# Optimization experiments

Hardware: AMD Instinct MI355X
Metric: run time of the kernel (lower is better)

The kernel has to match this reference:

```python
import jax, jax.numpy as jnp
import numpy as np

IM_SIZE = (256, 256)
OVERSAMP = 1.25
WIDTH = 6
BETA = float(np.pi * np.sqrt((WIDTH / OVERSAMP * (OVERSAMP - 0.5)) ** 2 - 0.8))
OS_SIZE = tuple(int(np.ceil(OVERSAMP * n)) for n in IM_SIZE)  # (320, 320)
D = 2


def _kb(x):
    # Kaiser-Bessel interpolation kernel: i0(beta*sqrt(1-x^2)) for |x|<=1 (sigpy convention)
    return jnp.i0(BETA * jnp.sqrt(jnp.maximum(1.0 - x * x, 0.0)))


def setup_inputs() -> dict:
    key = jax.random.key(0)
    k1, k2, k3 = jax.random.split(key, 3)
    N, C = 1, 8
    img_r = jax.random.normal(k1, (N, C) + IM_SIZE, dtype=jnp.float32)
    img_i = jax.random.normal(k2, (N, C) + IM_SIZE, dtype=jnp.float32)
    # trajectory in [-N_i/2, N_i/2] per the class docstring
    trj = (jax.random.uniform(k3, (N, 64, 4096, D), dtype=jnp.float32) - 0.5) * 256.0
    return {"img_r": img_r, "img_i": img_i, "trj": trj}


def _nufft_forward(img_r, img_i, trj):
    img = (img_r + 1j * img_i).astype(jnp.complex64)  # (N, C, H, W)
    nd = img.ndim
    # --- apodization (inverse FT of KB kernel), separable per axis ---
    for a in range(D):
        n, osn = IM_SIZE[a], OS_SIZE[a]
        idx = jnp.arange(n, dtype=jnp.float32)
        arg = jnp.sqrt(BETA ** 2 - (np.pi * WIDTH * (idx - n // 2) / osn) ** 2)
        apod = arg / jnp.sinh(arg)
        shape = [1] * nd
        shape[nd - D + a] = n
        img = img * apod.reshape(shape)
    # --- scale + centered zero-pad to oversampled grid ---
    img = img / np.sqrt(float(np.prod(IM_SIZE)))
    pads = [(0, 0)] * (nd - D) + [(((o - n) // 2), (o - n) - ((o - n) // 2))
                                  for n, o in zip(IM_SIZE, OS_SIZE)]
    img = jnp.pad(img, pads)
    # --- centered FFT (ifftshift -> fftn(norm=None) -> fftshift) ---
    axes = tuple(range(-D, 0))
    ksp_os = jnp.fft.fftshift(jnp.fft.fftn(jnp.fft.ifftshift(img, axes=axes), axes=axes), axes=axes)
    # --- scale trajectory to oversampled grid coordinates ---
    scale = jnp.array([OS_SIZE[a] / IM_SIZE[a] for a in range(D)], jnp.float32)
    shift = jnp.array([OS_SIZE[a] // 2 for a in range(D)], jnp.float32)
    coord = trj * scale + shift  # (N, R, S, 2)
    x0 = jnp.ceil(coord - WIDTH / 2.0)
    # --- KB interpolation: fixed 6x6 neighbor loop, vectorized gather over all points ---
    N = img.shape[0]
    out = jnp.zeros((N,) + img.shape[1:nd - D] + coord.shape[1:-1], jnp.complex64)

    def gather(grid, ix, iy):  # grid (C, Hos, Wos), ix/iy (R, S) -> (C, R, S)
        return grid[:, ix, iy]

    for dx in range(WIDTH):
        px = x0[..., 0] + dx
        wx = _kb((px - coord[..., 0]) / (WIDTH / 2.0))
        ix = px.astype(jnp.int32) % OS_SIZE[0]
        for dy in range(WIDTH):
            py = x0[..., 1] + dy
            wy = _kb((py - coord[..., 1]) / (WIDTH / 2.0))
            iy = py.astype(jnp.int32) % OS_SIZE[1]
            vals = jax.vmap(gather)(ksp_os, ix, iy)  # (N, C, R, S)
            out = out + vals * (wx * wy)[:, None, :, :]
    return out / (WIDTH ** D)


def reference(img_r, img_i, trj):
    return _nufft_forward(img_r, img_i, trj)
```

## Files before the change

### kernel.cpp

```cpp
#include <hip/hip_runtime.h>
#include <math.h>

#define NCH   8
#define IMN   256
#define OSN   320
#define NPTS  (64*4096)
#define KD    512
#define BETA_F   10.9551078f
#define BETA2_F  120.014389f
#define APOD_C   0.05890486225f

typedef unsigned short u16;
typedef unsigned int   u32;
typedef __attribute__((ext_vector_type(8))) short s16x8;
typedef __attribute__((ext_vector_type(4))) float f32x4;

__device__ __forceinline__ u32 f2bf(float f) {
    u32 u = __float_as_uint(f);
    return (u + 0x7FFFu + ((u >> 16) & 1u)) >> 16;
}

__device__ __forceinline__ float i0f(float t) {
    if (t < 3.75f) {
        float y = t * t * (1.0f / 14.0625f);
        return 1.0f + y * (3.5156229f + y * (3.0899424f + y * (1.2067492f +
                     y * (0.2659732f + y * (0.0360768f + y * 0.0045813f)))));
    }
    float z = 3.75f / t;
    float p = 0.39894228f + z * (0.01328592f + z * (0.00225319f + z * (-0.00157565f +
              z * (0.00916281f + z * (-0.02057706f + z * (0.02635537f +
              z * (-0.01647633f + z * 0.00392377f)))))));
    return expf(t) * rsqrtf(t) * p;
}

__device__ __forceinline__ float apodf(int i) {
    float x = APOD_C * (float)(i - IMN / 2);
    float arg = sqrtf(BETA2_F - x * x);
    float e = expf(arg);
    float sh = 0.5f * (e - 1.0f / e);
    return arg / sh;
}

__global__ void prep(const float* __restrict__ r, const float* __restrict__ im,
                     u32* __restrict__ B1, u32* __restrict__ B2,
                     u32* __restrict__ A) {
    const int b = blockIdx.x, t = threadIdx.x;
    if (b < (OSN * IMN) / 256) {
        int idx = b * 256 + t;
        int k = idx >> 8, j = idx & 255;
        int p = (k * (j + 32)) % OSN;
        float th = (2.0f * (float)M_PI / (float)OSN) * (float)p;
        float s = ((k + j) & 1) ? -1.0f : 1.0f;
        float sn, cs;
        sincosf(th, &sn, &cs);
        float re = s * cs, imv = -s * sn;
        B1[idx] = f2bf(re) | (f2bf(-imv) << 16);
        B2[idx] = f2bf(imv) | (f2bf(re) << 16);
    } else {
        int idx = (b - (OSN * IMN) / 256) * 256 + t;
        int i2 = idx & 255, i1 = (idx >> 8) & 255;
        float w = apodf(i1) * apodf(i2) * (1.0f / 256.0f);
        A[idx] = f2bf(r[idx] * w) | (f2bf(im[idx] * w) << 16);
    }
}

__launch_bounds__(64)
__global__ void gemm1(const short* __restrict__ Abf, const short* __restrict__ B1,
                      const short* __restrict__ B2, short* __restrict__ Tb) {
    const int c = blockIdx.z;
    const int mBase = blockIdx.y * 32;
    const int nBase = blockIdx.x * 32;
    __shared__ short As[2][32][36], B1s[2][32][36], B2s[2][32][36];
    const int t = threadIdx.x;
    const int row = t >> 1, seg = (t & 1) * 16;
    const int fm = t & 15, fq = (t >> 4) * 8;
    const short* ap  = Abf + (long)(c * IMN + mBase + row) * KD + seg;
    const short* b1p = B1 + (long)(nBase + row) * KD + seg;
    const short* b2p = B2 + (long)(nBase + row) * KD + seg;
    f32x4 zz = {0.f, 0.f, 0.f, 0.f};
    f32x4 accRe[2][2], accIm[2][2];
    #pragma unroll
    for (int i = 0; i < 2; i++)
        #pragma unroll
        for (int j = 0; j < 2; j++) { accRe[i][j] = zz; accIm[i][j] = zz; }

    s16x8 c0 = *(const s16x8*)(ap);
    s16x8 c1 = *(const s16x8*)(ap + 8);
    s16x8 c2 = *(const s16x8*)(b1p);
    s16x8 c3 = *(const s16x8*)(b1p + 8);
    s16x8 c4 = *(const s16x8*)(b2p);
    s16x8 c5 = *(const s16x8*)(b2p + 8);

    #pragma unroll
    for (int kc = 0; kc < 16; kc++) {
        const int buf = kc & 1;
        *(s16x8*)&As [buf][row][seg]     = c0;
        *(s16x8*)&As [buf][row][seg + 8] = c1;
        *(s16x8*)&B1s[buf][row][seg]     = c2;
        *(s16x8*)&B1s[buf][row][seg + 8] = c3;
        *(s16x8*)&B2s[buf][row][seg]     = c4;
        *(s16x8*)&B2s[buf][row][seg + 8] = c5;
        if (kc < 15) {
            const int kb = (kc + 1) * 32;
            c0 = *(const s16x8*)(ap + kb);
            c1 = *(const s16x8*)(ap + kb + 8);
            c2 = *(const s16x8*)(b1p + kb);
            c3 = *(const s16x8*)(b1p + kb + 8);
            c4 = *(const s16x8*)(b2p + kb);
            c5 = *(const s16x8*)(b2p + kb + 8);
        }
        s16x8 a0  = *(const s16x8*)&As [buf][fm][fq];
        s16x8 a1  = *(const s16x8*)&As [buf][16 + fm][fq];
        s16x8 b10 = *(const s16x8*)&B1s[buf][fm][fq];
        s16x8 b11 = *(const s16x8*)&B1s[buf][16 + fm][fq];
        s16x8 b20 = *(const s16x8*)&B2s[buf][fm][fq];
        s16x8 b21 = *(const s16x8*)&B2s[buf][16 + fm][fq];
        accRe[0][0] = __builtin_amdgcn_mfma_f32_16x16x32_bf16(a0, b10, accRe[0][0], 0, 0, 0);
        accRe[0][1] = __builtin_amdgcn_mfma_f32_16x16x32_bf16(a0, b11, accRe[0][1], 0, 0, 0);
        accRe[1][0] = __builtin_amdgcn_mfma_f32_16x16x32_bf16(a1, b10, accRe[1][0], 0, 0, 0);
        accRe[1][1] = __builtin_amdgcn_mfma_f32_16x16x32_bf16(a1, b11, accRe[1][1], 0, 0, 0);
        accIm[0][0] = __builtin_amdgcn_mfma_f32_16x16x32_bf16(a0, b20, accIm[0][0], 0, 0, 0);
        accIm[0][1] = __builtin_amdgcn_mfma_f32_16x16x32_bf16(a0, b21, accIm[0][1], 0, 0, 0);
        accIm[1][0] = __builtin_amdgcn_mfma_f32_16x16x32_bf16(a1, b20, accIm[1][0], 0, 0, 0);
        accIm[1][1] = __builtin_amdgcn_mfma_f32_16x16x32_bf16(a1, b21, accIm[1][1], 0, 0, 0);
    }
    #pragma unroll
    for (int i = 0; i < 2; i++)
        #pragma unroll
        for (int j = 0; j < 2; j++) {
            int i1b = mBase + i * 16 + (t >> 4) * 4;
            int k2  = nBase + j * 16 + fm;
            s16x8 v;
            #pragma unroll
            for (int r = 0; r < 4; r++) {
                v[2 * r]     = (short)f2bf(accRe[i][j][r]);
                v[2 * r + 1] = (short)f2bf(accIm[i][j][r]);
            }
            *(s16x8*)(Tb + ((long)(c * OSN + k2)) * KD + 2 * i1b) = v;
        }
}

__launch_bounds__(64)
__global__ void gemm2(const short* __restrict__ B1, const short* __restrict__ B2,
                      const short* __restrict__ Tb, u32* __restrict__ Gb) {
    const int c = blockIdx.z;
    const int mBase = blockIdx.y * 32;
    const int nBase = blockIdx.x * 32;
    __shared__ short A1s[2][32][36], A2s[2][32][36], Bs[2][32][36];
    const int t = threadIdx.x;
    const int row = t >> 1, seg = (t & 1) * 16;
    const int fm = t & 15, fq = (t >> 4) * 8;
    const short* a1p = B1 + (long)(mBase + row) * KD + seg;
    const short* a2p = B2 + (long)(mBase + row) * KD + seg;
    const short* bp  = Tb + ((long)(c * OSN + nBase + row)) * KD + seg;
    f32x4 zz = {0.f, 0.f, 0.f, 0.f};
    f32x4 accRe[2][2], accIm[2][2];
    #pragma unroll
    for (int i = 0; i < 2; i++)
        #pragma unroll
        for (int j = 0; j < 2; j++) { accRe[i][j] = zz; accIm[i][j] = zz; }

    s16x8 c0 = *(const s16x8*)(a1p);
    s16x8 c1 = *(const s16x8*)(a1p + 8);
    s16x8 c2 = *(const s16x8*)(a2p);
    s16x8 c3 = *(const s16x8*)(a2p + 8);
    s16x8 c4 = *(const s16x8*)(bp);
    s16x8 c5 = *(const s16x8*)(bp + 8);

    #pragma unroll
    for (int kc = 0; kc < 16; kc++) {
        const int buf = kc & 1;
        *(s16x8*)&A1s[buf][row][seg]     = c0;
        *(s16x8*)&A1s[buf][row][seg + 8] = c1;
        *(s16x8*)&A2s[buf][row][seg]     = c2;
        *(s16x8*)&A2s[buf][row][seg + 8] = c3;
        *(s16x8*)&Bs [buf][row][seg]     = c4;
        *(s16x8*)&Bs [buf][row][seg + 8] = c5;
        if (kc < 15) {
            const int kb = (kc + 1) * 32;
            c0 = *(const s16x8*)(a1p + kb);
            c1 = *(const s16x8*)(a1p + kb + 8);
            c2 = *(const s16x8*)(a2p + kb);
            c3 = *(const s16x8*)(a2p + kb + 8);
            c4 = *(const s16x8*)(bp + kb);
            c5 = *(const s16x8*)(bp + kb + 8);
        }
        s16x8 a10 = *(const s16x8*)&A1s[buf][fm][fq];
        s16x8 a11 = *(const s16x8*)&A1s[buf][16 + fm][fq];
        s16x8 a20 = *(const s16x8*)&A2s[buf][fm][fq];
        s16x8 a21 = *(const s16x8*)&A2s[buf][16 + fm][fq];
        s16x8 b0  = *(const s16x8*)&Bs [buf][fm][fq];
        s16x8 b1  = *(const s16x8*)&Bs [buf][16 + fm][fq];
        accRe[0][0] = __builtin_amdgcn_mfma_f32_16x16x32_bf16(a10, b0, accRe[0][0], 0, 0, 0);
        accRe[0][1] = __builtin_amdgcn_mfma_f32_16x16x32_bf16(a10, b1, accRe[0][1], 0, 0, 0);
        accRe[1][0] = __builtin_amdgcn_mfma_f32_16x16x32_bf16(a11, b0, accRe[1][0], 0, 0, 0);
        accRe[1][1] = __builtin_amdgcn_mfma_f32_16x16x32_bf16(a11, b1, accRe[1][1], 0, 0, 0);
        accIm[0][0] = __builtin_amdgcn_mfma_f32_16x16x32_bf16(a20, b0, accIm[0][0], 0, 0, 0);
        accIm[0][1] = __builtin_amdgcn_mfma_f32_16x16x32_bf16(a20, b1, accIm[0][1], 0, 0, 0);
        accIm[1][0] = __builtin_amdgcn_mfma_f32_16x16x32_bf16(a21, b0, accIm[1][0], 0, 0, 0);
        accIm[1][1] = __builtin_amdgcn_mfma_f32_16x16x32_bf16(a21, b1, accIm[1][1], 0, 0, 0);
    }
    #pragma unroll
    for (int i = 0; i < 2; i++)
        #pragma unroll
        for (int j = 0; j < 2; j++) {
            int k2 = nBase + j * 16 + fm;
            #pragma unroll
            for (int r = 0; r < 4; r++) {
                int k1 = mBase + i * 16 + (t >> 4) * 4 + r;
                Gb[((long)k1 * OSN + k2) * NCH + c] =
                    f2bf(accRe[i][j][r]) | (f2bf(accIm[i][j][r]) << 16);
            }
        }
}

__global__ void interp_kernel(const float* __restrict__ trj,
                              const u32* __restrict__ grid,
                              u32* __restrict__ out) {
    const int t = threadIdx.x;
    const int pl = t >> 2;
    const int cp = (t & 3) * 2;
    __shared__ float wxs[64][6], wys[64][6];
    __shared__ int   x0s[64], y0s[64];

    #pragma unroll
    for (int k = 0; k < 3; k++) {
        int e = t + 256 * k;
        int ptl = e / 12;
        int rem = e - ptl * 12;
        int axis = rem >= 6 ? 1 : 0;
        int d = rem - axis * 6;
        int pt = blockIdx.x * 64 + ptl;
        float tv = trj[pt * 2 + axis];
        float cc = __fadd_rn(__fmul_rn(tv, 1.25f), 160.0f);
        float v0 = ceilf(__fadd_rn(cc, -3.0f));
        if (d == 0) {
            if (axis) y0s[ptl] = (int)v0; else x0s[ptl] = (int)v0;
        }
        float u = __fdiv_rn(__fsub_rn(v0 + (float)d, cc), 3.0f);
        float wv = i0f(BETA_F * sqrtf(fmaxf(1.0f - u * u, 0.0f)));
        if (axis) wys[ptl][d] = wv; else wxs[ptl][d] = wv;
    }
    __syncthreads();

    int ix[6], iy[6];
    const int x0i = x0s[pl], y0i = y0s[pl];
    #pragma unroll
    for (int d = 0; d < 6; d++) {
        int vx = x0i + d;
        ix[d] = ((vx % OSN) + OSN) % OSN;
        int vy = y0i + d;
        iy[d] = ((vy % OSN) + OSN) % OSN;
    }

    float re0 = 0.f, im0 = 0.f, re1 = 0.f, im1 = 0.f;
    #pragma unroll
    for (int dx = 0; dx < 6; dx++) {
        long base = (long)ix[dx] * OSN;
        float wxv = wxs[pl][dx];
        #pragma unroll
        for (int dy = 0; dy < 6; dy++) {
            uint2 g = *(const uint2*)(grid + (base + iy[dy]) * NCH + cp);
            float ww = wxv * wys[pl][dy];
            re0 += __uint_as_float(g.x << 16) * ww;
            im0 += __uint_as_float(g.x & 0xFFFF0000u) * ww;
            re1 += __uint_as_float(g.y << 16) * ww;
            im1 += __uint_as_float(g.y & 0xFFFF0000u) * ww;
        }
    }
    re0 *= (1.0f / 36.0f); im0 *= (1.0f / 36.0f);
    re1 *= (1.0f / 36.0f); im1 *= (1.0f / 36.0f);

    __shared__ float2 lds[64 * 8];
    lds[pl * 8 + cp]     = make_float2(re0, im0);
    lds[pl * 8 + cp + 1] = make_float2(re1, im1);
    __syncthreads();
    int c2 = t >> 5, p2 = t & 31;
    float2 va = lds[p2 * 8 + c2];
    float2 vb = lds[(p2 + 32) * 8 + c2];
    long ob = (long)c2 * NPTS + blockIdx.x * 64;
    out[ob + p2]      = f2bf(va.y) | (f2bf(va.x) << 16);
    out[ob + p2 + 32] = f2bf(vb.y) | (f2bf(vb.x) << 16);
}

extern "C" void kernel_launch(void* const* d_in, const int* in_sizes, int n_in,
                              void* d_out, int out_size, void* d_ws, size_t ws_size,
                              hipStream_t stream) {
    const float* img_r = (const float*)d_in[0];
    const float* img_i = (const float*)d_in[1];
    const float* trj   = (const float*)d_in[2];

    char* ob = (char*)d_out;
    short* Tb  = (short*)(ob);
    u32*  B1u  = (u32*)(ob + 2621440);
    u32*  B2u  = (u32*)(ob + 2949120);
    u32*  Au   = (u32*)(ob + 3276800);
    u32*  Gb   = (u32*)d_ws;

    prep<<<(OSN * IMN) / 256 + (NCH * IMN * IMN) / 256, 256, 0, stream>>>(
        img_r, img_i, B1u, B2u, Au);
    gemm1<<<dim3(OSN / 32, IMN / 32, NCH), 64, 0, stream>>>(
        (const short*)Au, (const short*)B1u, (const short*)B2u, Tb);
    gemm2<<<dim3(OSN / 32, OSN / 32, NCH), 64, 0, stream>>>(
        (const short*)B1u, (const short*)B2u, Tb, Gb);
    interp_kernel<<<NPTS / 64, 256, 0, stream>>>(trj, Gb, (u32*)d_out);
}
```

Before: 111.9 us.

## Process 128 points per block with 16-byte grid gathers in interpolation

The interpolation kernel now assigns two threads per trajectory point, each loading four channels with a single 16-byte load, instead of four threads loading two channels each. Blocks cover 128 points. Kernel-weight computation is restructured so each thread computes all six weights for one axis. Modulo wrap is replaced by conditional add/subtract, offsets are precomputed as 32-bit integers, and accumulation uses packed float2 vectors. This is meant to cut the number of gather instructions and the index arithmetic per sample, at the cost of more registers per thread and fewer threads per point.

```diff
diff --git a/kernel.cpp b/kernel.cpp
--- a/kernel.cpp
+++ b/kernel.cpp
@@ -14,6 +14,7 @@
 typedef unsigned int   u32;
 typedef __attribute__((ext_vector_type(8))) short s16x8;
 typedef __attribute__((ext_vector_type(4))) float f32x4;
+typedef __attribute__((ext_vector_type(2))) float f32x2;
 
 __device__ __forceinline__ u32 f2bf(float f) {
     u32 u = __float_as_uint(f);
@@ -218,69 +219,80 @@
                               const u32* __restrict__ grid,
                               u32* __restrict__ out) {
     const int t = threadIdx.x;
-    const int pl = t >> 2;
-    const int cp = (t & 3) * 2;
-    __shared__ float wxs[64][6], wys[64][6];
-    __shared__ int   x0s[64], y0s[64];
-
-    #pragma unroll
-    for (int k = 0; k < 3; k++) {
-        int e = t + 256 * k;
-        int ptl = e / 12;
-        int rem = e - ptl * 12;
-        int axis = rem >= 6 ? 1 : 0;
-        int d = rem - axis * 6;
-        int pt = blockIdx.x * 64 + ptl;
+    __shared__ float wxs[128][6], wys[128][6];
+    __shared__ int   x0s[128], y0s[128];
+
+    {
+        int ptl = t & 127, axis = t >> 7;
+        int pt = blockIdx.x * 128 + ptl;
         float tv = trj[pt * 2 + axis];
         float cc = __fadd_rn(__fmul_rn(tv, 1.25f), 160.0f);
         float v0 = ceilf(__fadd_rn(cc, -3.0f));
-        if (d == 0) {
-            if (axis) y0s[ptl] = (int)v0; else x0s[ptl] = (int)v0;
-        }
-        float u = __fdiv_rn(__fsub_rn(v0 + (float)d, cc), 3.0f);
-        float wv = i0f(BETA_F * sqrtf(fmaxf(1.0f - u * u, 0.0f)));
-        if (axis) wys[ptl][d] = wv; else wxs[ptl][d] = wv;
+        if (axis) y0s[ptl] = (int)v0; else x0s[ptl] = (int)v0;
+        float* ws = axis ? wys[ptl] : wxs[ptl];
+        #pragma unroll
+        for (int d = 0; d < 6; d++) {
+            float u = __fdiv_rn(__fsub_rn(v0 + (float)d, cc), 3.0f);
+            ws[d] = i0f(BETA_F * sqrtf(fmaxf(1.0f - u * u, 0.0f)));
+        }
     }
     __syncthreads();
 
-    int ix[6], iy[6];
+    const int pl = t >> 1;
+    const int h = (t & 1) * 4;
+    int rb[6], iyb[6];
+    float wx[6], wy[6];
     const int x0i = x0s[pl], y0i = y0s[pl];
     #pragma unroll
     for (int d = 0; d < 6; d++) {
         int vx = x0i + d;
-        ix[d] = ((vx % OSN) + OSN) % OSN;
+        if (vx < 0) vx += OSN;
+        if (vx >= OSN) vx -= OSN;
+        rb[d] = vx * (OSN * NCH) + h;
         int vy = y0i + d;
-        iy[d] = ((vy % OSN) + OSN) % OSN;
-    }
-
-    float re0 = 0.f, im0 = 0.f, re1 = 0.f, im1 = 0.f;
+        if (vy < 0) vy += OSN;
+        if (vy >= OSN) vy -= OSN;
+        iyb[d] = vy * NCH;
+        wx[d] = wxs[pl][d];
+        wy[d] = wys[pl][d];
+    }
+
+    f32x2 a0 = {0.f, 0.f}, a1 = {0.f, 0.f}, a2 = {0.f, 0.f}, a3 = {0.f, 0.f};
     #pragma unroll
     for (int dx = 0; dx < 6; dx++) {
-        long base = (long)ix[dx] * OSN;
-        float wxv = wxs[pl][dx];
+        const u32* gp = grid + rb[dx];
+        float wxv = wx[dx];
         #pragma unroll
         for (int dy = 0; dy < 6; dy++) {
-            uint2 g = *(const uint2*)(grid + (base + iy[dy]) * NCH + cp);
-            float ww = wxv * wys[pl][dy];
-            re0 += __uint_as_float(g.x << 16) * ww;
-            im0 += __uint_as_float(g.x & 0xFFFF0000u) * ww;
-            re1 += __uint_as_float(g.y << 16) * ww;
-            im1 += __uint_as_float(g.y & 0xFFFF0000u) * ww;
-        }
-    }
-    re0 *= (1.0f / 36.0f); im0 *= (1.0f / 36.0f);
-    re1 *= (1.0f / 36.0f); im1 *= (1.0f / 36.0f);
-
-    __shared__ float2 lds[64 * 8];
-    lds[pl * 8 + cp]     = make_float2(re0, im0);
-    lds[pl * 8 + cp + 1] = make_float2(re1, im1);
+            uint4 g = *(const uint4*)(gp + iyb[dy]);
+            float ww = wxv * wy[dy];
+            f32x2 w2 = {ww, ww};
+            f32x2 v0v = { __uint_as_float(g.x << 16), __uint_as_float(g.x & 0xFFFF0000u) };
+            f32x2 v1v = { __uint_as_float(g.y << 16), __uint_as_float(g.y & 0xFFFF0000u) };
+            f32x2 v2v = { __uint_as_float(g.z << 16), __uint_as_float(g.z & 0xFFFF0000u) };
+            f32x2 v3v = { __uint_as_float(g.w << 16), __uint_as_float(g.w & 0xFFFF0000u) };
+            a0 += v0v * w2;
+            a1 += v1v * w2;
+            a2 += v2v * w2;
+            a3 += v3v * w2;
+        }
+    }
+    f32x2 sc = {1.0f / 36.0f, 1.0f / 36.0f};
+    a0 *= sc; a1 *= sc; a2 *= sc; a3 *= sc;
+
+    __shared__ f32x2 lds[128][8];
+    lds[pl][h]     = a0;
+    lds[pl][h + 1] = a1;
+    lds[pl][h + 2] = a2;
+    lds[pl][h + 3] = a3;
     __syncthreads();
     int c2 = t >> 5, p2 = t & 31;
-    float2 va = lds[p2 * 8 + c2];
-    float2 vb = lds[(p2 + 32) * 8 + c2];
-    long ob = (long)c2 * NPTS + blockIdx.x * 64;
-    out[ob + p2]      = f2bf(va.y) | (f2bf(va.x) << 16);
-    out[ob + p2 + 32] = f2bf(vb.y) | (f2bf(vb.x) << 16);
+    long ob = (long)c2 * NPTS + blockIdx.x * 128;
+    #pragma unroll
+    for (int k = 0; k < 4; k++) {
+        f32x2 v = lds[p2 + 32 * k][c2];
+        out[ob + p2 + 32 * k] = f2bf(v.y) | (f2bf(v.x) << 16);
+    }
 }
 
 extern "C" void kernel_launch(void* const* d_in, const int* in_sizes, int n_in,
@@ -303,5 +315,5 @@
         (const short*)Au, (const short*)B1u, (const short*)B2u, Tb);
     gemm2<<<dim3(OSN / 32, OSN / 32, NCH), 64, 0, stream>>>(
         (const short*)B1u, (const short*)B2u, Tb, Gb);
-    interp_kernel<<<NPTS / 64, 256, 0, stream>>>(trj, Gb, (u32*)d_out);
-}
+    interp_kernel<<<NPTS / 128, 256, 0, stream>>>(trj, Gb, (u32*)d_out);
+}
```

Result: slower. 119.4 us (+6.7%).
